# Performance work log

Hardware: AMD Instinct MI355X
Metric: run time of the kernel (lower is better)

## Reference

```python
import jax, jax.numpy as jnp
import numpy as np

B, NCAP, LV, LT, C = 64, 64, 197, 32, 512
NSP = LV - 1          # 196 spatial patches
NUM_KEEP = 98         # ceil(196 * sparse_ratio=0.5)
KEEPED = 49           # int(196 * aggr_ratio=0.5 * sparse_ratio=0.5)
HID = 102             # int(512 * dim_ratio=0.2)
LN_EPS = 1e-5


def _normalize(x):
    # torch F.normalize: x / max(||x||, 1e-12)
    return x / jnp.maximum(jnp.linalg.norm(x, axis=-1, keepdims=True), 1e-12)


def setup_inputs() -> dict:
    key = jax.random.key(0)
    ks = jax.random.split(key, 8)
    def rn(k, shape, s=0.02):
        return jax.random.normal(k, shape, jnp.float32) * s
    return {
        "img_embs": jax.random.normal(ks[0], (B, LV, C), jnp.float32),
        "cap_embs": jax.random.normal(ks[1], (NCAP, LT, C), jnp.float32),
        "cap_lens": jnp.full((NCAP,), LT, jnp.int32),
        "ln_gamma": jnp.ones((C,), jnp.float32),
        "ln_beta": jnp.zeros((C,), jnp.float32),
        "w1": rn(ks[2], (C, HID)), "b1": jnp.zeros((HID,), jnp.float32),
        "w2": rn(ks[3], (HID, KEEPED)), "b2": jnp.zeros((KEEPED,), jnp.float32),
        "aggr_scale": jnp.ones((1, 1, 1), jnp.float32),
        "wi2t": rn(ks[4], (C, C)), "bi2t": jnp.zeros((C,), jnp.float32),
        "wt2i": rn(ks[5], (C, C)), "bt2i": jnp.zeros((C,), jnp.float32),
        "temp": jnp.ones((1, 1, 1), jnp.float32),
    }


def _forward(img_embs, cap_embs, ln_gamma, ln_beta, w1, b1, w2, b2,
             aggr_scale, wi2t, bi2t, wt2i, bt2i, temp):
    img_norm = _normalize(img_embs)
    img_cls = img_embs[:, 0:1]              # [B,1,C]  has_cls_token branch
    img_sp = img_embs[:, 1:]                # [B,196,C]
    img_sp_norm = img_norm[:, 1:]
    # use_cls_as_glob_embd: global = normalized CLS (no grad)
    glo = jax.lax.stop_gradient(img_norm[:, 0:1])
    attn_x = jax.lax.stop_gradient(jnp.sum(glo * img_sp_norm, -1))  # [B,196]
    cap_norm = _normalize(cap_embs)
    bidx = jnp.arange(B)[:, None]

    def ln(x):
        m = x.mean(-1, keepdims=True)
        v = jnp.var(x, axis=-1, keepdims=True)
        return (x - m) / jnp.sqrt(v + LN_EPS) * ln_gamma + ln_beta

    def per_caption(cap_i, cap_i_norm):
        # cap_i, cap_i_norm: [LT, C]
        cap_glo = jax.lax.stop_gradient(_normalize(cap_i[0:1]))           # [1,C]
        attn_y = jax.lax.stop_gradient(jnp.sum(cap_glo[None] * img_sp_norm, -1))  # [B,196]
        # --- TokenSparse ---
        score = attn_x + attn_y
        order = jnp.argsort(-score, axis=1)                              # descending
        keep, nonkeep = order[:, :NUM_KEEP], order[:, NUM_KEEP:]
        sel = img_sp[bidx, keep]                                          # [B,98,C]
        non = img_sp[bidx, nonkeep]                                       # [B,98,C]
        non_score = jnp.take_along_axis(score, nonkeep, 1)
        extra = jnp.sum(non * jax.nn.softmax(non_score, axis=1)[..., None],
                        axis=1, keepdims=True)                            # [B,1,C]
        # --- TokenAggregation ---
        h = jax.nn.gelu(ln(sel) @ w1 + b1, approximate=False)             # [B,98,HID]
        w = jnp.swapaxes(h @ w2 + b2, 1, 2) * aggr_scale                  # [B,49,98]
        aggr = jax.nn.softmax(w, axis=2) @ sel                            # [B,49,C]
        # [cls, aggr, extra] -> [B,51,C], then normalize
        sel_tok = _normalize(jnp.concatenate([img_cls, aggr, extra], 1))
        Ls = sel_tok.shape[1]
        # --- 'attn' similarity ---
        cap_exp = jnp.broadcast_to(cap_i_norm[None], (B, LT, C))
        st = jnp.swapaxes(sel_tok, 1, 2)                                  # [B,C,51]
        c2i = jax.nn.leaky_relu(cap_exp @ st, negative_slope=0.1)         # [B,LT,51]
        a_i2t = jax.nn.softmax((cap_exp @ wi2t + bi2t) @ st / temp, axis=1)
        a_t2i = jax.nn.softmax((cap_exp @ wt2i + bt2i) @ st / temp, axis=2)
        return jnp.sum(a_i2t * c2i / Ls + a_t2i * c2i / LT, axis=(1, 2))  # [B]

    sims = jax.vmap(per_caption)(cap_embs, cap_norm)                      # [NCAP,B]
    return sims.T                                                         # [B,NCAP]


def reference(img_embs, cap_embs, cap_lens, ln_gamma, ln_beta, w1, b1, w2, b2,
              aggr_scale, wi2t, bi2t, wt2i, bt2i, temp):
    # cap_lens are all LT (static shapes); eval-mode output: similarity matrix.
    return _forward(img_embs, cap_embs, ln_gamma, ln_beta, w1, b1, w2, b2,
                    aggr_scale, wi2t, bi2t, wt2i, bt2i, temp)
```

## Files before the change

### kernel.cpp

```cpp
#include <hip/hip_runtime.h>
#include <math.h>

#define B     64
#define NCAP  64
#define LV    197
#define LT    32
#define C     512
#define NSP   196
#define NKEEP 98
#define HID   102
#define KEEPED 49

#define OFF_ATTNX   12608
#define OFF_WSMAT   25152
#define OFF_WT      639808
#define OFF_GLOT    1688384
#define OFF_ATTNYT  1721152
#define OFF_IMGT    14164800
#define OFF_QBB     17834816
#define OFF_QCAP    19407680

typedef unsigned int u32;
typedef unsigned short u16;
typedef __bf16 bf16x8 __attribute__((ext_vector_type(8)));
typedef float f32x4 __attribute__((ext_vector_type(4)));
typedef unsigned int uint4v __attribute__((ext_vector_type(4)));

__device__ __forceinline__ u16 f2bf(float f) {
    u32 u = __builtin_bit_cast(u32, f);
    return (u16)((u + 0x7FFFu + ((u >> 16) & 1u)) >> 16);
}
__device__ __forceinline__ bf16x8 ld_bf8(const u16* p) {
    uint4v v = *reinterpret_cast<const uint4v*>(p);
    return __builtin_bit_cast(bf16x8, v);
}

__device__ __forceinline__ float gelu_exact(float x) {
    return 0.5f * x * (1.f + erff(x * 0.70710678118654752f));
}

__global__ __launch_bounds__(256) void k_pre(const float* __restrict__ img,
                                             const float* __restrict__ cap,
                                             const float* __restrict__ wi2t,
                                             const float* __restrict__ wt2i,
                                             u16* __restrict__ imgTf,
                                             float* __restrict__ gloT,
                                             u16* __restrict__ Qbbf,
                                             u16* __restrict__ Qcap,
                                             u16* __restrict__ wT) {
    int idx = blockIdx.x, t = threadIdx.x;
    __shared__ __align__(16) u16 shb[64 * 224];

    if (idx < 512) {
        int b = idx >> 3, cg = idx & 7;
        for (int f = t; f < 64 * 27; f += 256) shb[(f / 27) * 224 + 197 + (f % 27)] = 0;
        int cc = t & 63;
        for (int sb = t >> 6; sb < 197; sb += 4) {
            float v = img[((size_t)b * LV + sb) * C + cg * 64 + cc];
            shb[cc * 224 + sb] = f2bf(v);
        }
        __syncthreads();
        const u32* Tu = (const u32*)shb;
        u32* outp = (u32*)imgTf + (size_t)b * 7 * 32 * 256;
        for (int f = t; f < 7 * 4 * 256; f += 256) {
            int ks = f >> 10, rem = f & 1023;
            int ctl = rem >> 8, g = rem & 255;
            int lane_o = g >> 2, j2 = g & 3;
            int quad_o = lane_o >> 4, l15_o = lane_o & 15;
            int ccl = ctl * 16 + l15_o;
            int s = ks * 32 + quad_o * 8 + 2 * j2;
            u32 v = Tu[ccl * 112 + (s >> 1)];
            outp[(size_t)(ks * 32 + cg * 4 + ctl) * 256 + g] = v;
        }
    } else if (idx < 1024) {
        int e = idx - 512, i = e >> 3, tg = e & 7;
        int lane = t & 63, wv = t >> 6;
        int tt = tg * 4 + wv;
        const float* row = cap + ((size_t)i * LT + tt) * C;
        float v[8]; float ss = 0.f;
#pragma unroll
        for (int q = 0; q < 8; ++q) { v[q] = row[lane + 64 * q]; ss += v[q] * v[q]; }
        for (int o = 32; o > 0; o >>= 1) ss += __shfl_down(ss, o);
        ss = __shfl(ss, 0);
        float inv = 1.f / fmaxf(sqrtf(ss), 1e-12f);
        u16* qrow = Qcap + ((size_t)i * 32 + tt) * C;
        int mi = tt >> 4, l15f = tt & 15;
        u16* qfb = Qbbf + (size_t)(i * 6 + mi) * 16 * 512;
#pragma unroll
        for (int q = 0; q < 8; ++q) {
            float n = v[q] * inv;
            u16 nb = f2bf(n);
            int c = lane + 64 * q;
            qrow[c] = nb;
            int ks = c >> 5, quadf = (c >> 3) & 3, jf = c & 7;
            qfb[(size_t)ks * 512 + (quadf * 16 + l15f) * 8 + jf] = nb;
            if (tt == 0) gloT[c * NCAP + i] = n;
        }
    } else {
        int e = idx - 1024;
        int mat = e >> 6, ty = e & 63, jg = ty >> 3, cg = ty & 7;
        const float* W = mat ? wt2i : wi2t;
        u16 (*tile)[65] = (u16(*)[65])shb;
        for (int f = t; f < 4096; f += 256) {
            int cc2 = f >> 6, jj = f & 63;
            tile[jj][cc2] = f2bf(W[(size_t)(cg * 64 + cc2) * 512 + jg * 64 + jj]);
        }
        __syncthreads();
        for (int f = t; f < 4096; f += 256) {
            int jj = f >> 6, cc2 = f & 63;
            wT[((size_t)mat * 512 + jg * 64 + jj) * 512 + cg * 64 + cc2] = tile[jj][cc2];
        }
    }
}

__global__ __launch_bounds__(512) void k_mid(const float* __restrict__ img,
                                             const u16* __restrict__ wT,
                                             const float* __restrict__ bi2t,
                                             const float* __restrict__ bt2i,
                                             const u16* __restrict__ Qcap,
                                             u16* __restrict__ Qbbf,
                                             const float* __restrict__ gamw,
                                             const float* __restrict__ betw,
                                             const float* __restrict__ w1,
                                             const float* __restrict__ b1,
                                             const float* __restrict__ w2,
                                             const float* __restrict__ b2,
                                             const float* __restrict__ scale_p,
                                             const float* __restrict__ gloT,
                                             float* __restrict__ attn_x,
                                             float* __restrict__ WsM,
                                             float* __restrict__ attn_yT) {
    int idx = blockIdx.x, t = threadIdx.x;
    __shared__ __align__(16) float shm[4960 + 16];

    if (idx < 256) {
        int i = idx & 63, p = idx >> 6;
        int lane = t & 63, wu = t >> 6;
        int l15 = lane & 15, quad = lane >> 4;
        int mat = wu >> 2;
        int miq = (wu >> 1) & 1;
        int nh  = wu & 1;
        int ni0 = p * 8 + nh * 4;
        const u16* Arow = Qcap + ((size_t)i * 32 + miq * 16 + l15) * 512;
        const u16* Wm   = wT + (size_t)mat * 512 * 512;
        f32x4 acc[4];
#pragma unroll
        for (int n = 0; n < 4; ++n) acc[n] = (f32x4){0.f, 0.f, 0.f, 0.f};
        bf16x8 A = ld_bf8(Arow + quad * 8);
        bf16x8 Bf[4];
#pragma unroll
        for (int n = 0; n < 4; ++n)
            Bf[n] = ld_bf8(Wm + (size_t)((ni0 + n) * 16 + l15) * 512 + quad * 8);
        for (int ks = 0; ks < 16; ++ks) {
            bf16x8 An; bf16x8 Bn[4];
            if (ks < 15) {
                An = ld_bf8(Arow + (ks + 1) * 32 + quad * 8);
#pragma unroll
                for (int n = 0; n < 4; ++n)
                    Bn[n] = ld_bf8(Wm + (size_t)((ni0 + n) * 16 + l15) * 512 + (ks + 1) * 32 + quad * 8);
            }
#pragma unroll
            for (int n = 0; n < 4; ++n)
                acc[n] = __builtin_amdgcn_mfma_f32_16x16x32_bf16(A, Bf[n], acc[n], 0, 0, 0);
            A = An;
#pragma unroll
            for (int n = 0; n < 4; ++n) Bf[n] = Bn[n];
        }
        const float* bias = mat ? bt2i : bi2t;
#pragma unroll
        for (int n = 0; n < 4; ++n) {
            int j = (ni0 + n) * 16 + l15;
            float bj = bias[j];
            int ksf = j >> 5, quadf = (j >> 3) & 3, jf = j & 7;
#pragma unroll
            for (int r = 0; r < 4; ++r) {
                int q = 32 + mat * 32 + miq * 16 + quad * 4 + r;
                int mi = q >> 4, l15f = q & 15;
                Qbbf[(size_t)((i * 6 + mi) * 16 + ksf) * 512 + (quadf * 16 + l15f) * 8 + jf]
                    = f2bf(acc[n][r] + bj);
            }
        }
    } else if (idx < 1856) {
        int e = idx - 256;
        int b = e / 25, sg = e - b * 25;
        int s0 = sg * 8;
        int R = NSP - s0; if (R > 8) R = 8;
        float (*lnr)[C]   = (float(*)[C])shm;
        float (*HH)[104]  = (float(*)[104])(shm + 4096);
        float (*redm)[4]  = (float(*)[4])(shm + 4928);

        int g = t >> 6, lane = t & 63;
        if (g < R) {
            const float* row = img + ((size_t)b * LV + 1 + s0 + g) * C;
            const float* cls = img + (size_t)b * LV * C;
            float sm = 0.f, ss = 0.f, dd = 0.f, sc = 0.f;
            for (int c = lane; c < C; c += 64) {
                float v = row[c];
                float cv = cls[c];
                sm += v; ss += v * v; dd += v * cv; sc += cv * cv;
                lnr[g][c] = v;
            }
            for (int o = 32; o > 0; o >>= 1) {
                sm += __shfl_down(sm, o);
                ss += __shfl_down(ss, o);
                dd += __shfl_down(dd, o);
                sc += __shfl_down(sc, o);
            }
            if (lane == 0) { redm[g][0] = sm; redm[g][1] = ss; redm[g][2] = dd; redm[g][3] = sc; }
        }
        __syncthreads();
        for (int f = t; f < R * C; f += 512) {
            int rr = f >> 9, c = f & 511;
            float mean = redm[rr][0] * (1.f / C);
            float var  = redm[rr][1] * (1.f / C) - mean * mean;
            float rstd = 1.f / sqrtf(var + 1e-5f);
            lnr[rr][c] = (lnr[rr][c] - mean) * rstd * gamw[c] + betw[c];
        }
        if (t < R) {
            float inv0 = 1.f / fmaxf(sqrtf(redm[t][3]), 1e-12f);
            float invs = 1.f / fmaxf(sqrtf(redm[t][1]), 1e-12f);
            attn_x[b * NSP + s0 + t] = redm[t][2] * inv0 * invs;
        }
        __syncthreads();
        if (t < 408) {
            int rr2 = t / 102;
            int j = t - rr2 * 102;
            int rw0 = rr2 * 2, rw1 = rr2 * 2 + 1;
            float a0 = b1[j], a1 = b1[j];
            for (int c = 0; c < C; ++c) {
                float wv = w1[c * HID + j];
                a0 += lnr[rw0][c] * wv;
                a1 += lnr[rw1][c] * wv;
            }
            if (rw0 < R) HH[rw0][j] = gelu_exact(a0);
            if (rw1 < R) HH[rw1][j] = gelu_exact(a1);
        }
        __syncthreads();
        float scale = scale_p[0];
        if (t < 392) {
            int k = t % 49, rh = t / 49;
            if (rh < R) {
                float a = b2[k];
                for (int h = 0; h < HID; ++h) a += HH[rh][h] * w2[h * 49 + k];
                WsM[((size_t)b * NSP + s0 + rh) * 49 + k] = a * scale;
            }
        }
    } else {
        int e = idx - 1856;
        int b = e / 25;
        int s0 = (e - b * 25) * 8;
        int R = NSP - s0; if (R > 8) R = 8;
        float (*xr)[C] = (float(*)[C])shm;
        float* rnorm = shm + 4096;

        for (int f = t; f < R * C; f += 512) {
            int rr = f >> 9, c = f & 511;
            xr[rr][c] = img[((size_t)b * LV + 1 + s0 + rr) * C + c];
        }
        __syncthreads();
        {
            int row = t >> 6, l = t & 63;
            if (row < R) {
                float ss = 0.f;
                for (int c = l; c < C; c += 64) { float v = xr[row][c]; ss += v * v; }
                for (int o = 32; o > 0; o >>= 1) ss += __shfl_down(ss, o);
                if (l == 0) rnorm[row] = 1.f / fmaxf(sqrtf(ss), 1e-12f);
            }
        }
        __syncthreads();
        for (int f = t; f < R * C; f += 512) {
            int rr = f >> 9, c = f & 511;
            xr[rr][c] *= rnorm[rr];
        }
        __syncthreads();
        int i = t & 63, w = t >> 6;
        if (w < R) {
            float a0 = 0.f;
            for (int c4 = 0; c4 < C / 4; ++c4) {
                float g0 = gloT[(c4 * 4 + 0) * NCAP + i];
                float g1 = gloT[(c4 * 4 + 1) * NCAP + i];
                float g2 = gloT[(c4 * 4 + 2) * NCAP + i];
                float g3 = gloT[(c4 * 4 + 3) * NCAP + i];
                float4 x0 = ((const float4*)xr[w])[c4];
                a0 += x0.x * g0 + x0.y * g1 + x0.z * g2 + x0.w * g3;
            }
            attn_yT[((size_t)b * NCAP + i) * NSP + s0 + w] = a0;
        }
    }
}

__global__ __launch_bounds__(512, 4) void k_main(const float* __restrict__ attn_x,
                                                 const float* __restrict__ attn_yT,
                                                 const float* __restrict__ WsM,
                                                 const u16* __restrict__ imgTf,
                                                 const u16* __restrict__ Qbbf,
                                                 const float* __restrict__ temp_p,
                                                 float* __restrict__ out) {
    int lin = blockIdx.x + NCAP * blockIdx.y;
    int b = (lin & 7) * 8 + ((lin >> 3) & 7);
    int i = lin >> 6;
    int t = threadIdx.x;
    int lane = t & 63, wu = t >> 6;
    int l15 = lane & 15, quad = lane >> 4;

    __shared__ __align__(16) u16 TnBuf[51 * 520];
    __shared__ float rowsq[8][64];
    __shared__ float invn[64];
    __shared__ float colM[51], colZ[51], rowM[32], rowZ[32], redw[8];
    __shared__ float scoreS[NSP];
    __shared__ int   keepL[NKEEP];
    __shared__ int   nonL[NKEEP];
    __shared__ float snon[NKEEP];
    __shared__ short rnkH[2][NSP];

    u16*   Pf   = TnBuf;
    float* ULDS = (float*)TnBuf;

    {
        u32* Pfu = (u32*)Pf;
        for (int f = t; f < 51 * 116; f += 512) Pfu[f] = 0;
    }
    if (t < NSP)
        scoreS[t] = attn_x[b * NSP + t] + attn_yT[((size_t)b * NCAP + i) * NSP + t];
    __syncthreads();
    if (t < 2 * NSP) {
        int half = (t >= NSP) ? 1 : 0;
        int s = t - half * NSP;
        float sv = scoreS[s];
        int u0 = half * 98, u1 = half ? NSP : 98;
        int r = 0;
        for (int u = u0; u < u1; ++u) {
            float o = scoreS[u];
            r += (o > sv) || (o == sv && u < s);
        }
        rnkH[half][s] = (short)r;
    }
    __syncthreads();
    if (t < NSP) {
        int r = rnkH[0][t] + rnkH[1][t];
        if (r < NKEEP) keepL[r] = t;
        else { nonL[r - NKEEP] = t; snon[r - NKEEP] = scoreS[t]; }
    }
    __syncthreads();
    if (t == 0) Pf[0] = 0x3F80;
    for (int f = t; f < NKEEP * KEEPED; f += 512) {
        int j = f / KEEPED, k = f - j * KEEPED;
        int s = keepL[j];
        Pf[(1 + k) * 232 + 1 + s] = f2bf(expf(WsM[((size_t)b * NSP + s) * KEEPED + k]));
    }
    if (t < NKEEP) Pf[50 * 232 + 1 + nonL[t]] = f2bf(expf(snon[t]));
    __syncthreads();

    const u16* imgTb = imgTf + (size_t)b * 7 * 32 * 512;
    f32x4 acc[4][4];
#pragma unroll
    for (int mi = 0; mi < 4; ++mi)
#pragma unroll
        for (int nj = 0; nj < 4; ++nj) acc[mi][nj] = (f32x4){0.f, 0.f, 0.f, 0.f};

    for (int ks = 0; ks < 7; ++ks) {
        bf16x8 Afr[4];
#pragma unroll
        for (int mi = 0; mi < 4; ++mi)
            Afr[mi] = ld_bf8(Pf + (mi * 16 + l15) * 232 + ks * 32 + quad * 8);
#pragma unroll
        for (int nj = 0; nj < 4; ++nj) {
            bf16x8 Bf = ld_bf8(imgTb + (size_t)(ks * 32 + wu * 4 + nj) * 512 + lane * 8);
#pragma unroll
            for (int mi = 0; mi < 4; ++mi)
                acc[mi][nj] = __builtin_amdgcn_mfma_f32_16x16x32_bf16(Afr[mi], Bf, acc[mi][nj], 0, 0, 0);
        }
    }

#pragma unroll
    for (int mi = 0; mi < 4; ++mi)
#pragma unroll
        for (int r = 0; r < 4; ++r) {
            float s = acc[mi][0][r] * acc[mi][0][r] + acc[mi][1][r] * acc[mi][1][r]
                    + acc[mi][2][r] * acc[mi][2][r] + acc[mi][3][r] * acc[mi][3][r];
            s += __shfl_down(s, 8); s += __shfl_down(s, 4);
            s += __shfl_down(s, 2); s += __shfl_down(s, 1);
            if (l15 == 0) rowsq[wu][mi * 16 + quad * 4 + r] = s;
        }
    __syncthreads();
    if (t < 64) {
        float s = 0.f;
#pragma unroll
        for (int w2 = 0; w2 < 8; ++w2) s += rowsq[w2][t];
        invn[t] = 1.f / fmaxf(sqrtf(s), 1e-12f);
    }
    __syncthreads();

#pragma unroll
    for (int mi = 0; mi < 4; ++mi)
#pragma unroll
        for (int r = 0; r < 4; ++r) {
            int row = mi * 16 + quad * 4 + r;
            if (row < 51) {
                float iv = invn[row];
#pragma unroll
                for (int nj = 0; nj < 4; ++nj)
                    TnBuf[row * 520 + (wu * 4 + nj) * 16 + l15] = f2bf(acc[mi][nj][r] * iv);
            }
        }
    __syncthreads();

    const u16* Qbf = Qbbf + (size_t)i * 6 * 16 * 512;
    f32x4 ua[3];
#pragma unroll
    for (int e = 0; e < 3; ++e) ua[e] = (f32x4){0.f, 0.f, 0.f, 0.f};

    if (wu < 6) {
        int mi = wu;
        const u16* Ar = Qbf + (size_t)mi * 16 * 512 + lane * 8;
        bf16x8 Af = ld_bf8(Ar);
        for (int ks = 0; ks < 16; ++ks) {
            bf16x8 An;
            if (ks < 15) An = ld_bf8(Ar + (ks + 1) * 512);
#pragma unroll
            for (int e = 0; e < 3; ++e) {
                bf16x8 Bf = ld_bf8(TnBuf + (e * 16 + l15) * 520 + ks * 32 + quad * 8);
                ua[e] = __builtin_amdgcn_mfma_f32_16x16x32_bf16(Af, Bf, ua[e], 0, 0, 0);
            }
            Af = An;
        }
    } else {
        int w2 = wu - 6;
        int rowB = 48 + l15; if (rowB > 50) rowB = 50;
        const u16* Ar0 = Qbf + (size_t)(3 * w2 + 0) * 16 * 512 + lane * 8;
        const u16* Ar1 = Qbf + (size_t)(3 * w2 + 1) * 16 * 512 + lane * 8;
        const u16* Ar2 = Qbf + (size_t)(3 * w2 + 2) * 16 * 512 + lane * 8;
        bf16x8 Af0 = ld_bf8(Ar0);
        bf16x8 Af1 = ld_bf8(Ar1);
        bf16x8 Af2 = ld_bf8(Ar2);
        for (int ks = 0; ks < 16; ++ks) {
            bf16x8 An0, An1, An2;
            if (ks < 15) {
                An0 = ld_bf8(Ar0 + (ks + 1) * 512);
                An1 = ld_bf8(Ar1 + (ks + 1) * 512);
                An2 = ld_bf8(Ar2 + (ks + 1) * 512);
            }
            bf16x8 Bf = ld_bf8(TnBuf + rowB * 520 + ks * 32 + quad * 8);
            ua[0] = __builtin_amdgcn_mfma_f32_16x16x32_bf16(Af0, Bf, ua[0], 0, 0, 0);
            ua[1] = __builtin_amdgcn_mfma_f32_16x16x32_bf16(Af1, Bf, ua[1], 0, 0, 0);
            ua[2] = __builtin_amdgcn_mfma_f32_16x16x32_bf16(Af2, Bf, ua[2], 0, 0, 0);
            Af0 = An0; Af1 = An1; Af2 = An2;
        }
    }
    __syncthreads();

    if (wu < 6) {
#pragma unroll
        for (int e = 0; e < 3; ++e) {
            int l = e * 16 + l15;
            int q0 = wu * 16 + quad * 4;
#pragma unroll
            for (int r = 0; r < 4; ++r) ULDS[(q0 + r) * 52 + l] = ua[e][r];
        }
    } else {
        int l = 48 + l15;
        if (l < 51) {
            int w2 = wu - 6;
#pragma unroll
            for (int e = 0; e < 3; ++e) {
                int q0 = (3 * w2 + e) * 16 + quad * 4;
#pragma unroll
                for (int r = 0; r < 4; ++r) ULDS[(q0 + r) * 52 + l] = ua[e][r];
            }
        }
    }
    __syncthreads();

    float invT = 1.f / temp_p[0];
    if (t < 51) {
        float mm = -1e30f;
        for (int u = 0; u < LT; ++u) mm = fmaxf(mm, ULDS[(32 + u) * 52 + t] * invT);
        float z = 0.f;
        for (int u = 0; u < LT; ++u) z += expf(ULDS[(32 + u) * 52 + t] * invT - mm);
        colM[t] = mm; colZ[t] = 1.f / z;
    }
    if (t >= 64 && t < 96) {
        int u = t - 64;
        float mm = -1e30f;
        for (int l = 0; l < 51; ++l) mm = fmaxf(mm, ULDS[(64 + u) * 52 + l] * invT);
        float z = 0.f;
        for (int l = 0; l < 51; ++l) z += expf(ULDS[(64 + u) * 52 + l] * invT - mm);
        rowM[u] = mm; rowZ[u] = 1.f / z;
    }
    __syncthreads();

    float part = 0.f;
    for (int f = t; f < LT * 51; f += 512) {
        int u = f / 51, l = f - u * 51;
        float u0 = ULDS[u * 52 + l];
        float c2 = (u0 > 0.f) ? u0 : 0.1f * u0;
        float av = expf(ULDS[(32 + u) * 52 + l] * invT - colM[l]) * colZ[l];
        float bv = expf(ULDS[(64 + u) * 52 + l] * invT - rowM[u]) * rowZ[u];
        part += c2 * (av * (1.f / 51.f) + bv * (1.f / 32.f));
    }
    for (int o = 32; o > 0; o >>= 1) part += __shfl_down(part, o);
    if (lane == 0) redw[wu] = part;
    __syncthreads();
    if (t == 0) {
        float s = 0.f;
#pragma unroll
        for (int w2 = 0; w2 < 8; ++w2) s += redw[w2];
        out[b * NCAP + i] = s;
    }
}

extern "C" void kernel_launch(void* const* d_in, const int* in_sizes, int n_in,
                              void* d_out, int out_size, void* d_ws, size_t ws_size,
                              hipStream_t stream) {
    const float* img        = (const float*)d_in[0];
    const float* cap        = (const float*)d_in[1];
    const float* gamw       = (const float*)d_in[3];
    const float* betw       = (const float*)d_in[4];
    const float* w1         = (const float*)d_in[5];
    const float* b1         = (const float*)d_in[6];
    const float* w2         = (const float*)d_in[7];
    const float* b2         = (const float*)d_in[8];
    const float* aggr_scale = (const float*)d_in[9];
    const float* wi2t       = (const float*)d_in[10];
    const float* bi2t       = (const float*)d_in[11];
    const float* wt2i       = (const float*)d_in[12];
    const float* bt2i       = (const float*)d_in[13];
    const float* temp       = (const float*)d_in[14];
    float* out = (float*)d_out;

    float* ws      = (float*)d_ws;
    float* attn_x  = ws + OFF_ATTNX;
    float* WsM     = ws + OFF_WSMAT;
    u16*   wT      = (u16*)(ws + OFF_WT);
    float* gloT    = ws + OFF_GLOT;
    float* attn_yT = ws + OFF_ATTNYT;
    u16*   imgTf   = (u16*)(ws + OFF_IMGT);
    u16*   Qbbf    = (u16*)(ws + OFF_QBB);
    u16*   Qcap    = (u16*)(ws + OFF_QCAP);

    k_pre<<<dim3(1152), dim3(256), 0, stream>>>(img, cap, wi2t, wt2i, imgTf, gloT, Qbbf, Qcap, wT);
    k_mid<<<dim3(3456), dim3(512), 0, stream>>>(img, wT, bi2t, bt2i, Qcap, Qbbf, gamw, betw,
                                                w1, b1, w2, b2, aggr_scale, gloT,
                                                attn_x, WsM, attn_yT);
    k_main<<<dim3(NCAP, B), dim3(512), 0, stream>>>(attn_x, attn_yT, WsM, imgTf, Qbbf, temp, out);
}
```

Measured before the change: 429.9 us.

## Move LN/MLP score branch into k_pre and parallelize softmax stats

Moves the per-patch LayerNorm/MLP weight-matrix work (attn_x, WsM), which has no dependency on earlier-stage outputs, from the middle kernel into the first kernel. The first kernel now runs at 512 threads, so its other branches are re-split to match. This rebalances work across the three launches and shrinks the middle kernel's grid. In k_main, the column and row softmax max/sum reductions now use 8 lanes per row or column with shuffle reductions instead of one serial thread each, and the LDS zero-fill uses 16-byte stores. The changes add more LDS pressure in k_pre, and the re-split shifts load balance.

```diff
diff --git a/kernel.cpp b/kernel.cpp
--- a/kernel.cpp
+++ b/kernel.cpp
@@ -39,30 +39,40 @@
     return 0.5f * x * (1.f + erff(x * 0.70710678118654752f));
 }
 
-__global__ __launch_bounds__(256) void k_pre(const float* __restrict__ img,
+__global__ __launch_bounds__(512) void k_pre(const float* __restrict__ img,
                                              const float* __restrict__ cap,
                                              const float* __restrict__ wi2t,
                                              const float* __restrict__ wt2i,
+                                             const float* __restrict__ gamw,
+                                             const float* __restrict__ betw,
+                                             const float* __restrict__ w1,
+                                             const float* __restrict__ b1,
+                                             const float* __restrict__ w2,
+                                             const float* __restrict__ b2,
+                                             const float* __restrict__ scale_p,
                                              u16* __restrict__ imgTf,
                                              float* __restrict__ gloT,
                                              u16* __restrict__ Qbbf,
                                              u16* __restrict__ Qcap,
-                                             u16* __restrict__ wT) {
+                                             u16* __restrict__ wT,
+                                             float* __restrict__ attn_x,
+                                             float* __restrict__ WsM) {
     int idx = blockIdx.x, t = threadIdx.x;
-    __shared__ __align__(16) u16 shb[64 * 224];
+    __shared__ __align__(16) u16 shbu[64 * 224];
+    float* shm = (float*)shbu;
 
     if (idx < 512) {
         int b = idx >> 3, cg = idx & 7;
-        for (int f = t; f < 64 * 27; f += 256) shb[(f / 27) * 224 + 197 + (f % 27)] = 0;
+        for (int f = t; f < 64 * 27; f += 512) shbu[(f / 27) * 224 + 197 + (f % 27)] = 0;
         int cc = t & 63;
-        for (int sb = t >> 6; sb < 197; sb += 4) {
+        for (int sb = t >> 6; sb < 197; sb += 8) {
             float v = img[((size_t)b * LV + sb) * C + cg * 64 + cc];
-            shb[cc * 224 + sb] = f2bf(v);
-        }
-        __syncthreads();
-        const u32* Tu = (const u32*)shb;
+            shbu[cc * 224 + sb] = f2bf(v);
+        }
+        __syncthreads();
+        const u32* Tu = (const u32*)shbu;
         u32* outp = (u32*)imgTf + (size_t)b * 7 * 32 * 256;
-        for (int f = t; f < 7 * 4 * 256; f += 256) {
+        for (int f = t; f < 7 * 4 * 256; f += 512) {
             int ks = f >> 10, rem = f & 1023;
             int ctl = rem >> 8, g = rem & 255;
             int lane_o = g >> 2, j2 = g & 3;
@@ -72,10 +82,10 @@
             u32 v = Tu[ccl * 112 + (s >> 1)];
             outp[(size_t)(ks * 32 + cg * 4 + ctl) * 256 + g] = v;
         }
-    } else if (idx < 1024) {
-        int e = idx - 512, i = e >> 3, tg = e & 7;
+    } else if (idx < 768) {
+        int e = idx - 512, i = e >> 2, tg = e & 3;
         int lane = t & 63, wv = t >> 6;
-        int tt = tg * 4 + wv;
+        int tt = tg * 8 + wv;
         const float* row = cap + ((size_t)i * LT + tt) * C;
         float v[8]; float ss = 0.f;
 #pragma unroll
@@ -96,42 +106,98 @@
             qfb[(size_t)ks * 512 + (quadf * 16 + l15f) * 8 + jf] = nb;
             if (tt == 0) gloT[c * NCAP + i] = n;
         }
-    } else {
-        int e = idx - 1024;
+    } else if (idx < 896) {
+        int e = idx - 768;
         int mat = e >> 6, ty = e & 63, jg = ty >> 3, cg = ty & 7;
         const float* W = mat ? wt2i : wi2t;
-        u16 (*tile)[65] = (u16(*)[65])shb;
-        for (int f = t; f < 4096; f += 256) {
+        u16 (*tile)[65] = (u16(*)[65])shbu;
+        for (int f = t; f < 4096; f += 512) {
             int cc2 = f >> 6, jj = f & 63;
             tile[jj][cc2] = f2bf(W[(size_t)(cg * 64 + cc2) * 512 + jg * 64 + jj]);
         }
         __syncthreads();
-        for (int f = t; f < 4096; f += 256) {
+        for (int f = t; f < 4096; f += 512) {
             int jj = f >> 6, cc2 = f & 63;
             wT[((size_t)mat * 512 + jg * 64 + jj) * 512 + cg * 64 + cc2] = tile[jj][cc2];
         }
-    }
-}
-
-__global__ __launch_bounds__(512) void k_mid(const float* __restrict__ img,
-                                             const u16* __restrict__ wT,
-                                             const float* __restrict__ bi2t,
-                                             const float* __restrict__ bt2i,
-                                             const u16* __restrict__ Qcap,
-                                             u16* __restrict__ Qbbf,
-                                             const float* __restrict__ gamw,
-                                             const float* __restrict__ betw,
-                                             const float* __restrict__ w1,
-                                             const float* __restrict__ b1,
-                                             const float* __restrict__ w2,
-                                             const float* __restrict__ b2,
-                                             const float* __restrict__ scale_p,
-                                             const float* __restrict__ gloT,
-                                             float* __restrict__ attn_x,
-                                             float* __restrict__ WsM,
-                                             float* __restrict__ attn_yT) {
+    } else {
+        int e = idx - 896;
+        int b = e / 25, sg = e - b * 25;
+        int s0 = sg * 8;
+        int R = NSP - s0; if (R > 8) R = 8;
+        float (*lnr)[C]   = (float(*)[C])shm;
+        float (*HH)[104]  = (float(*)[104])(shm + 4096);
+        float (*redm)[4]  = (float(*)[4])(shm + 4928);
+
+        int g = t >> 6, lane = t & 63;
+        if (g < R) {
+            const float* row = img + ((size_t)b * LV + 1 + s0 + g) * C;
+            const float* cls = img + (size_t)b * LV * C;
+            float sm = 0.f, ss = 0.f, dd = 0.f, sc = 0.f;
+            for (int c = lane; c < C; c += 64) {
+                float v = row[c];
+                float cv = cls[c];
+                sm += v; ss += v * v; dd += v * cv; sc += cv * cv;
+                lnr[g][c] = v;
+            }
+            for (int o = 32; o > 0; o >>= 1) {
+                sm += __shfl_down(sm, o);
+                ss += __shfl_down(ss, o);
+                dd += __shfl_down(dd, o);
+                sc += __shfl_down(sc, o);
+            }
+            if (lane == 0) { redm[g][0] = sm; redm[g][1] = ss; redm[g][2] = dd; redm[g][3] = sc; }
+        }
+        __syncthreads();
+        for (int f = t; f < R * C; f += 512) {
+            int rr = f >> 9, c = f & 511;
+            float mean = redm[rr][0] * (1.f / C);
+            float var  = redm[rr][1] * (1.f / C) - mean * mean;
+            float rstd = 1.f / sqrtf(var + 1e-5f);
+            lnr[rr][c] = (lnr[rr][c] - mean) * rstd * gamw[c] + betw[c];
+        }
+        if (t < R) {
+            float inv0 = 1.f / fmaxf(sqrtf(redm[t][3]), 1e-12f);
+            float invs = 1.f / fmaxf(sqrtf(redm[t][1]), 1e-12f);
+            attn_x[b * NSP + s0 + t] = redm[t][2] * inv0 * invs;
+        }
+        __syncthreads();
+        if (t < 408) {
+            int rr2 = t / 102;
+            int j = t - rr2 * 102;
+            int rw0 = rr2 * 2, rw1 = rr2 * 2 + 1;
+            float a0 = b1[j], a1 = b1[j];
+            for (int c = 0; c < C; ++c) {
+                float wv = w1[c * HID + j];
+                a0 += lnr[rw0][c] * wv;
+                a1 += lnr[rw1][c] * wv;
+            }
+            if (rw0 < R) HH[rw0][j] = gelu_exact(a0);
+            if (rw1 < R) HH[rw1][j] = gelu_exact(a1);
+        }
+        __syncthreads();
+        float scale = scale_p[0];
+        if (t < 392) {
+            int k = t % 49, rh = t / 49;
+            if (rh < R) {
+                float a = b2[k];
+                for (int h = 0; h < HID; ++h) a += HH[rh][h] * w2[h * 49 + k];
+                WsM[((size_t)b * NSP + s0 + rh) * 49 + k] = a * scale;
+            }
+        }
+    }
+}
+
+__global__ __launch_bounds__(512) void k_mid2(const float* __restrict__ img,
+                                              const u16* __restrict__ wT,
+                                              const float* __restrict__ bi2t,
+                                              const float* __restrict__ bt2i,
+                                              const u16* __restrict__ Qcap,
+                                              u16* __restrict__ Qbbf,
+                                              const float* __restrict__ gloT,
+                                              float* __restrict__ attn_yT) {
     int idx = blockIdx.x, t = threadIdx.x;
-    __shared__ __align__(16) float shm[4960 + 16];
+    __shared__ __align__(16) float shm[4160];
 
     if (idx < 256) {
         int i = idx & 63, p = idx >> 6;
@@ -180,73 +246,8 @@
                     = f2bf(acc[n][r] + bj);
             }
         }
-    } else if (idx < 1856) {
+    } else {
         int e = idx - 256;
-        int b = e / 25, sg = e - b * 25;
-        int s0 = sg * 8;
-        int R = NSP - s0; if (R > 8) R = 8;
-        float (*lnr)[C]   = (float(*)[C])shm;
-        float (*HH)[104]  = (float(*)[104])(shm + 4096);
-        float (*redm)[4]  = (float(*)[4])(shm + 4928);
-
-        int g = t >> 6, lane = t & 63;
-        if (g < R) {
-            const float* row = img + ((size_t)b * LV + 1 + s0 + g) * C;
-            const float* cls = img + (size_t)b * LV * C;
-            float sm = 0.f, ss = 0.f, dd = 0.f, sc = 0.f;
-            for (int c = lane; c < C; c += 64) {
-                float v = row[c];
-                float cv = cls[c];
-                sm += v; ss += v * v; dd += v * cv; sc += cv * cv;
-                lnr[g][c] = v;
-            }
-            for (int o = 32; o > 0; o >>= 1) {
-                sm += __shfl_down(sm, o);
-                ss += __shfl_down(ss, o);
-                dd += __shfl_down(dd, o);
-                sc += __shfl_down(sc, o);
-            }
-            if (lane == 0) { redm[g][0] = sm; redm[g][1] = ss; redm[g][2] = dd; redm[g][3] = sc; }
-        }
-        __syncthreads();
-        for (int f = t; f < R * C; f += 512) {
-            int rr = f >> 9, c = f & 511;
-            float mean = redm[rr][0] * (1.f / C);
-            float var  = redm[rr][1] * (1.f / C) - mean * mean;
-            float rstd = 1.f / sqrtf(var + 1e-5f);
-            lnr[rr][c] = (lnr[rr][c] - mean) * rstd * gamw[c] + betw[c];
-        }
-        if (t < R) {
-            float inv0 = 1.f / fmaxf(sqrtf(redm[t][3]), 1e-12f);
-            float invs = 1.f / fmaxf(sqrtf(redm[t][1]), 1e-12f);
-            attn_x[b * NSP + s0 + t] = redm[t][2] * inv0 * invs;
-        }
-        __syncthreads();
-        if (t < 408) {
-            int rr2 = t / 102;
-            int j = t - rr2 * 102;
-            int rw0 = rr2 * 2, rw1 = rr2 * 2 + 1;
-            float a0 = b1[j], a1 = b1[j];
-            for (int c = 0; c < C; ++c) {
-                float wv = w1[c * HID + j];
-                a0 += lnr[rw0][c] * wv;
-                a1 += lnr[rw1][c] * wv;
-            }
-            if (rw0 < R) HH[rw0][j] = gelu_exact(a0);
-            if (rw1 < R) HH[rw1][j] = gelu_exact(a1);
-        }
-        __syncthreads();
-        float scale = scale_p[0];
-        if (t < 392) {
-            int k = t % 49, rh = t / 49;
-            if (rh < R) {
-                float a = b2[k];
-                for (int h = 0; h < HID; ++h) a += HH[rh][h] * w2[h * 49 + k];
-                WsM[((size_t)b * NSP + s0 + rh) * 49 + k] = a * scale;
-            }
-        }
-    } else {
-        int e = idx - 1856;
         int b = e / 25;
         int s0 = (e - b * 25) * 8;
         int R = NSP - s0; if (R > 8) R = 8;
@@ -317,8 +318,8 @@
     float* ULDS = (float*)TnBuf;
 
     {
-        u32* Pfu = (u32*)Pf;
-        for (int f = t; f < 51 * 116; f += 512) Pfu[f] = 0;
+        uint4v* Pfv = (uint4v*)Pf;
+        for (int f = t; f < 51 * 232 / 8; f += 512) Pfv[f] = (uint4v){0, 0, 0, 0};
     }
     if (t < NSP)
         scoreS[t] = attn_x[b * NSP + t] + attn_yT[((size_t)b * NCAP + i) * NSP + t];
@@ -472,20 +473,39 @@
     __syncthreads();
 
     float invT = 1.f / temp_p[0];
-    if (t < 51) {
-        float mm = -1e30f;
-        for (int u = 0; u < LT; ++u) mm = fmaxf(mm, ULDS[(32 + u) * 52 + t] * invT);
+    if (t < 408) {
+        int l = t >> 3, sub = t & 7;
+        float vbuf[4]; float mm = -1e30f;
+#pragma unroll
+        for (int q = 0; q < 4; ++q) {
+            float v = ULDS[(32 + sub + 8 * q) * 52 + l] * invT;
+            vbuf[q] = v;
+            mm = fmaxf(mm, v);
+        }
+#pragma unroll
+        for (int o = 1; o < 8; o <<= 1) mm = fmaxf(mm, __shfl_xor(mm, o, 8));
         float z = 0.f;
-        for (int u = 0; u < LT; ++u) z += expf(ULDS[(32 + u) * 52 + t] * invT - mm);
-        colM[t] = mm; colZ[t] = 1.f / z;
-    }
-    if (t >= 64 && t < 96) {
-        int u = t - 64;
-        float mm = -1e30f;
-        for (int l = 0; l < 51; ++l) mm = fmaxf(mm, ULDS[(64 + u) * 52 + l] * invT);
+#pragma unroll
+        for (int q = 0; q < 4; ++q) z += expf(vbuf[q] - mm);
+#pragma unroll
+        for (int o = 1; o < 8; o <<= 1) z += __shfl_xor(z, o, 8);
+        if (sub == 0) { colM[l] = mm; colZ[l] = 1.f / z; }
+    }
+    if (t < 256) {
+        int u = t >> 3, sub = t & 7;
+        float vbuf[7]; int cnt = 0; float mm = -1e30f;
+        for (int l = sub; l < 51; l += 8) {
+            float v = ULDS[(64 + u) * 52 + l] * invT;
+            vbuf[cnt++] = v;
+            mm = fmaxf(mm, v);
+        }
+#pragma unroll
+        for (int o = 1; o < 8; o <<= 1) mm = fmaxf(mm, __shfl_xor(mm, o, 8));
         float z = 0.f;
-        for (int l = 0; l < 51; ++l) z += expf(ULDS[(64 + u) * 52 + l] * invT - mm);
-        rowM[u] = mm; rowZ[u] = 1.f / z;
+        for (int q = 0; q < cnt; ++q) z += expf(vbuf[q] - mm);
+#pragma unroll
+        for (int o = 1; o < 8; o <<= 1) z += __shfl_xor(z, o, 8);
+        if (sub == 0) { rowM[u] = mm; rowZ[u] = 1.f / z; }
     }
     __syncthreads();
 
@@ -538,9 +558,11 @@
     u16*   Qbbf    = (u16*)(ws + OFF_QBB);
     u16*   Qcap    = (u16*)(ws + OFF_QCAP);
 
-    k_pre<<<dim3(1152), dim3(256), 0, stream>>>(img, cap, wi2t, wt2i, imgTf, gloT, Qbbf, Qcap, wT);
-    k_mid<<<dim3(3456), dim3(512), 0, stream>>>(img, wT, bi2t, bt2i, Qcap, Qbbf, gamw, betw,
-                                                w1, b1, w2, b2, aggr_scale, gloT,
-                                                attn_x, WsM, attn_yT);
+    k_pre<<<dim3(2496), dim3(512), 0, stream>>>(img, cap, wi2t, wt2i, gamw, betw,
+                                                w1, b1, w2, b2, aggr_scale,
+                                                imgTf, gloT, Qbbf, Qcap, wT,
+                                                attn_x, WsM);
+    k_mid2<<<dim3(1856), dim3(512), 0, stream>>>(img, wT, bi2t, bt2i, Qcap, Qbbf,
+                                                 gloT, attn_yT);
     k_main<<<dim3(NCAP, B), dim3(512), 0, stream>>>(attn_x, attn_yT, WsM, imgTf, Qbbf, temp, out);
 }
```

Measured after the change: 440.1 us. 1.02x slower.
